# Kernel tuning notes

Measured on AMD Instinct MI355X. Metric: run time of the kernel, lower is better.

Reference implementation:

```python
import jax, jax.numpy as jnp
import numpy as np
from jax import lax

L, H = 16384, 1024
EPS = 1e-5


def _ln(x, w, b):
    m = jnp.mean(x, axis=-1, keepdims=True)
    v = jnp.var(x, axis=-1, keepdims=True)
    return (x - m) * lax.rsqrt(v + EPS) * w + b


def setup_inputs() -> dict:
    key = jax.random.key(0)
    ks = jax.random.split(key, 12)
    s = 0.02
    return {
        "x": jax.random.normal(ks[0], (L, H), dtype=jnp.float32),
        "ln1_w": jnp.ones((H,), jnp.float32),
        "ln1_b": jnp.zeros((H,), jnp.float32),
        "W_in": jax.random.normal(ks[1], (H, H), jnp.float32) * s,
        "b_in": jnp.zeros((H,), jnp.float32),
        "W_gate": jax.random.normal(ks[2], (H, H), jnp.float32) * s,
        "b_gate": jnp.zeros((H,), jnp.float32),
        "W_out": jax.random.normal(ks[3], (H, H), jnp.float32) * s,
        "b_out": jnp.zeros((H,), jnp.float32),
        "state_decay": jnp.zeros((H,), jnp.float32),
        "ln2_w": jnp.ones((H,), jnp.float32),
        "ln2_b": jnp.zeros((H,), jnp.float32),
        "W_ff1": jax.random.normal(ks[4], (H, 2 * H), jnp.float32) * s,
        "b_ff1": jnp.zeros((2 * H,), jnp.float32),
        "W_ff2": jax.random.normal(ks[5], (2 * H, H), jnp.float32) * s,
        "b_ff2": jnp.zeros((H,), jnp.float32),
    }


def reference(x, ln1_w, ln1_b, W_in, b_in, W_gate, b_gate, W_out, b_out,
              state_decay, ln2_w, ln2_b, W_ff1, b_ff1, W_ff2, b_ff2):
    hidden = _ln(x, ln1_w, ln1_b)                       # [L,H]
    u = hidden @ W_in + b_in                            # [L,H]
    gate = jax.nn.sigmoid(hidden @ W_gate + b_gate)     # [L,H]
    decay = jax.nn.sigmoid(state_decay)                 # [H]

    def step(s, u_t):
        s = decay * s + u_t
        return s, s

    z = jnp.zeros((x.shape[1],), x.dtype)
    _, states_f = lax.scan(step, z, u)                  # forward recurrence
    _, states_b = lax.scan(step, z, u, reverse=True)    # backward recurrence
    state_out = 0.5 * (states_f + states_b) * gate

    x = x + state_out @ W_out + b_out
    h = _ln(x, ln2_w, ln2_b)
    x = x + jax.nn.silu(h @ W_ff1 + b_ff1) @ W_ff2 + b_ff2
    return x
```

## Files before the change

kernel.cpp:

```cpp
#include <hip/hip_runtime.h>
#include <hip/hip_bf16.h>
#include <hip/hip_fp16.h>

#define L_SEQ 16384
#define HDIM  1024
#define CH    32
#define NC    (L_SEQ / CH)

typedef _Float16 f16;
typedef _Float16 f16x8 __attribute__((ext_vector_type(8)));
typedef _Float16 f16x4 __attribute__((ext_vector_type(4)));
typedef float    f32x4 __attribute__((ext_vector_type(4)));

#define AS1(p) (const __attribute__((address_space(1))) void*)(p)
#define AS3(p) (__attribute__((address_space(3))) void*)(p)

__global__ __launch_bounds__(256) void wcvt_t(const float* __restrict__ in,
                                              f16* __restrict__ out, int K, int N) {
  __shared__ float tile[32][33];
  int n0 = blockIdx.x * 32, k0 = blockIdx.y * 32;
  int tx = threadIdx.x, ty = threadIdx.y;
#pragma unroll
  for (int i = 0; i < 4; i++) {
    int k = k0 + ty + i * 8;
    tile[ty + i * 8][tx] = in[(size_t)k * N + n0 + tx];
  }
  __syncthreads();
#pragma unroll
  for (int i = 0; i < 4; i++) {
    int n = n0 + ty + i * 8;
    out[(size_t)n * K + k0 + tx] = (f16)tile[tx][ty + i * 8];
  }
}

__global__ __launch_bounds__(256) void ln_k(const float* __restrict__ x,
                                            const float* __restrict__ w,
                                            const float* __restrict__ b,
                                            f16* __restrict__ out,
                                            f16* __restrict__ xcopy) {
  int row = blockIdx.x;
  int t = threadIdx.x;
  const float4* xr = (const float4*)(x + (size_t)row * HDIM);
  float4 v = xr[t];
  float s  = v.x + v.y + v.z + v.w;
  float s2 = v.x * v.x + v.y * v.y + v.z * v.z + v.w * v.w;
#pragma unroll
  for (int off = 32; off > 0; off >>= 1) {
    s  += __shfl_down(s, off);
    s2 += __shfl_down(s2, off);
  }
  __shared__ float red[8];
  int wid = t >> 6, lane = t & 63;
  if (lane == 0) { red[wid] = s; red[4 + wid] = s2; }
  __syncthreads();
  if (t == 0) {
    red[0] = red[0] + red[1] + red[2] + red[3];
    red[4] = red[4] + red[5] + red[6] + red[7];
  }
  __syncthreads();
  float mean = red[0] * (1.0f / HDIM);
  float var  = red[4] * (1.0f / HDIM) - mean * mean;
  float rstd = rsqrtf(var + 1e-5f);
  float4 ww = ((const float4*)w)[t];
  float4 bb = ((const float4*)b)[t];
  f16x4 o;
  o[0] = (f16)((v.x - mean) * rstd * ww.x + bb.x);
  o[1] = (f16)((v.y - mean) * rstd * ww.y + bb.y);
  o[2] = (f16)((v.z - mean) * rstd * ww.z + bb.z);
  o[3] = (f16)((v.w - mean) * rstd * ww.w + bb.w);
  ((f16x4*)(out + (size_t)row * HDIM))[t] = o;
  if (xcopy) {
    f16x4 c;
    c[0] = (f16)v.x; c[1] = (f16)v.y; c[2] = (f16)v.z; c[3] = (f16)v.w;
    ((f16x4*)(xcopy + (size_t)row * HDIM))[t] = c;
  }
}

__global__ __launch_bounds__(128) void ln_k16(const f16* __restrict__ x,
                                              const float* __restrict__ w,
                                              const float* __restrict__ b,
                                              f16* __restrict__ out) {
  int row = blockIdx.x;
  int t = threadIdx.x;
  f16x8 xv = ((const f16x8*)(x + (size_t)row * HDIM))[t];
  float v[8];
  float s = 0.f, s2 = 0.f;
#pragma unroll
  for (int i = 0; i < 8; i++) {
    v[i] = (float)xv[i];
    s += v[i]; s2 += v[i] * v[i];
  }
#pragma unroll
  for (int off = 32; off > 0; off >>= 1) {
    s  += __shfl_down(s, off);
    s2 += __shfl_down(s2, off);
  }
  __shared__ float red[4];
  int wid = t >> 6, lane = t & 63;
  if (lane == 0) { red[wid] = s; red[2 + wid] = s2; }
  __syncthreads();
  float mean = (red[0] + red[1]) * (1.0f / HDIM);
  float var  = (red[2] + red[3]) * (1.0f / HDIM) - mean * mean;
  float rstd = rsqrtf(var + 1e-5f);
  float4 w1 = ((const float4*)w)[2 * t], w2 = ((const float4*)w)[2 * t + 1];
  float4 b1 = ((const float4*)b)[2 * t], b2 = ((const float4*)b)[2 * t + 1];
  float wv[8] = {w1.x, w1.y, w1.z, w1.w, w2.x, w2.y, w2.z, w2.w};
  float bv[8] = {b1.x, b1.y, b1.z, b1.w, b2.x, b2.y, b2.z, b2.w};
  f16x8 o;
#pragma unroll
  for (int i = 0; i < 8; i++) o[i] = (f16)((v[i] - mean) * rstd * wv[i] + bv[i]);
  ((f16x8*)(out + (size_t)row * HDIM))[t] = o;
}

template <int MODE, int RESID, int OUTF16>
__global__ __launch_bounds__(256, 4) void gemm_bt(const f16* __restrict__ A,
                                                  const f16* __restrict__ BT,
                                                  const float* __restrict__ bias,
                                                  const float* __restrict__ bias2,
                                                  const f16* __restrict__ resid,
                                                  void* __restrict__ Cout,
                                                  void* __restrict__ Cout2,
                                                  int M, int N, int K) {
  __shared__ __align__(16) f16 As[2][128 * 32];
  __shared__ __align__(16) f16 Bs[2][128 * 32];
  const int tid  = threadIdx.x;
  const int lane = tid & 63, wid = tid >> 6;
  const int wm = wid >> 1, wn = wid & 1;
  const int quad = lane >> 4, l16 = lane & 15;

  const int nbx = N >> 7, nby = M >> 7;
  const int b = blockIdx.x;
  const int xcd = b & 7;
  const int i = b >> 3;
  const int strips = nby >> 3;
  const int rs = i / nbx, cb = i - rs * nbx;
  const long m0 = (long)(xcd * strips + rs) << 7;
  const long n0 = (long)cb << 7;

  const int srow = wid * 16 + (lane >> 2);
  const int scol = (lane & 3) * 8;
  const f16* gA = A  + (m0 + srow) * K + scol;
  const f16* gB = BT + (n0 + srow) * K + scol;
  const int sdst = wid * 1024;

  f32x4 zero = {0.f, 0.f, 0.f, 0.f};
  f32x4 acc[4][4];
#pragma unroll
  for (int i2 = 0; i2 < 4; i2++)
#pragma unroll
    for (int j = 0; j < 4; j++) acc[i2][j] = zero;

#pragma unroll
  for (int it = 0; it < 2; ++it) {
    __builtin_amdgcn_global_load_lds(AS1(gA + (size_t)(it * 64) * K),
                                     AS3((char*)As[0] + it * 4096 + sdst), 16, 0, 0);
    __builtin_amdgcn_global_load_lds(AS1(gB + (size_t)(it * 64) * K),
                                     AS3((char*)Bs[0] + it * 4096 + sdst), 16, 0, 0);
  }
  __syncthreads();

  const int niter = K >> 5;
  for (int ki = 0; ki < niter; ++ki) {
    const int cur = ki & 1;
    if (ki + 1 < niter) {
      const int nxt = cur ^ 1;
      const int koff = (ki + 1) << 5;
#pragma unroll
      for (int it = 0; it < 2; ++it) {
        __builtin_amdgcn_global_load_lds(AS1(gA + (size_t)(it * 64) * K + koff),
                                         AS3((char*)As[nxt] + it * 4096 + sdst), 16, 0, 0);
        __builtin_amdgcn_global_load_lds(AS1(gB + (size_t)(it * 64) * K + koff),
                                         AS3((char*)Bs[nxt] + it * 4096 + sdst), 16, 0, 0);
      }
    }
    f16x8 af[4], bfr[4];
#pragma unroll
    for (int mi = 0; mi < 4; ++mi)
      af[mi] = *(const f16x8*)(As[cur] + (wm * 64 + mi * 16 + l16) * 32 + quad * 8);
#pragma unroll
    for (int ni = 0; ni < 4; ++ni)
      bfr[ni] = *(const f16x8*)(Bs[cur] + (wn * 64 + ni * 16 + l16) * 32 + quad * 8);
#pragma unroll
    for (int mi = 0; mi < 4; ++mi)
#pragma unroll
      for (int ni = 0; ni < 4; ++ni)
        acc[mi][ni] = __builtin_amdgcn_mfma_f32_16x16x32_f16(af[mi], bfr[ni], acc[mi][ni], 0, 0, 0);
    __syncthreads();
  }

#pragma unroll
  for (int mi = 0; mi < 4; ++mi) {
#pragma unroll
    for (int ni = 0; ni < 4; ++ni) {
      const long col = n0 + wn * 64 + ni * 16 + l16;
      float bc;
      if (MODE == 3) bc = (col < HDIM) ? bias[col] : bias2[col - HDIM];
      else           bc = bias[col];
#pragma unroll
      for (int r = 0; r < 4; ++r) {
        const long row = m0 + wm * 64 + mi * 16 + quad * 4 + r;
        float v = acc[mi][ni][r] + bc;
        if (MODE == 2) v = v / (1.f + __expf(-v));
        if (MODE == 3) {
          if (col < HDIM) {
            ((f16*)Cout)[row * HDIM + col] = (f16)v;
          } else {
            float g = 1.f / (1.f + __expf(-v));
            ((f16*)Cout2)[row * HDIM + (col - HDIM)] = (f16)g;
          }
        } else {
          if (RESID) v += (float)resid[row * N + col];
          if (OUTF16) ((f16*)Cout)[row * N + col] = (f16)v;
          else        ((float*)Cout)[row * N + col] = v;
        }
      }
    }
  }
}

__global__ __launch_bounds__(256) void scan_p1(const f16* __restrict__ u,
                                               const float* __restrict__ sdecay,
                                               float* __restrict__ carry_f,
                                               float* __restrict__ carry_b) {
  int tid = blockIdx.x * 256 + threadIdx.x;
  int h = tid & (HDIM - 1);
  int c = tid >> 10;
  float d = 1.f / (1.f + expf(-sdecay[h]));
  const f16* up = u + (size_t)c * CH * HDIM + h;
  float sf = 0.f, sb = 0.f, p = 1.f;
#pragma unroll
  for (int i = 0; i < CH; i++) {
    float uu = (float)up[i * HDIM];
    sf = d * sf + uu;
    sb += p * uu;
    p *= d;
  }
  carry_f[(size_t)c * HDIM + h] = sf;
  carry_b[(size_t)c * HDIM + h] = sb;
}

__global__ __launch_bounds__(256) void scan_p2(const float* __restrict__ sdecay,
                                               const float* __restrict__ carry_f,
                                               const float* __restrict__ carry_b,
                                               float* __restrict__ cin_f,
                                               float* __restrict__ cin_b) {
  int tid = blockIdx.x * 256 + threadIdx.x;
  int h = tid & (HDIM - 1);
  int dir = tid >> 10;
  float d = 1.f / (1.f + expf(-sdecay[h]));
  float dT = powf(d, (float)CH);
  float S = 0.f;
  if (dir == 0) {
#pragma unroll 4
    for (int c = 0; c < NC; c++) {
      cin_f[(size_t)c * HDIM + h] = S;
      S = dT * S + carry_f[(size_t)c * HDIM + h];
    }
  } else {
#pragma unroll 4
    for (int c = NC - 1; c >= 0; c--) {
      cin_b[(size_t)c * HDIM + h] = S;
      S = dT * S + carry_b[(size_t)c * HDIM + h];
    }
  }
}

__global__ __launch_bounds__(256) void scan_p3(const f16* __restrict__ u,
                                               const f16* __restrict__ gate,
                                               const float* __restrict__ sdecay,
                                               const float* __restrict__ cin_f,
                                               const float* __restrict__ cin_b,
                                               f16* __restrict__ state_out) {
  int tid = blockIdx.x * 256 + threadIdx.x;
  int h = tid & (HDIM - 1);
  int c = tid >> 10;
  float d = 1.f / (1.f + expf(-sdecay[h]));
  const f16* up = u    + (size_t)c * CH * HDIM + h;
  const f16* gp = gate + (size_t)c * CH * HDIM + h;
  f16* op = state_out  + (size_t)c * CH * HDIM + h;
  float ur[CH], sf[CH];
#pragma unroll
  for (int i = 0; i < CH; i++) ur[i] = (float)up[i * HDIM];
  float s = cin_f[(size_t)c * HDIM + h];
#pragma unroll
  for (int i = 0; i < CH; i++) { s = d * s + ur[i]; sf[i] = s; }
  s = cin_b[(size_t)c * HDIM + h];
#pragma unroll
  for (int i = CH - 1; i >= 0; i--) {
    s = d * s + ur[i];
    float g = (float)gp[i * HDIM];
    op[i * HDIM] = (f16)(0.5f * (sf[i] + s) * g);
  }
}

extern "C" void kernel_launch(void* const* d_in, const int* in_sizes, int n_in,
                              void* d_out, int out_size, void* d_ws, size_t ws_size,
                              hipStream_t stream) {
  const float* x      = (const float*)d_in[0];
  const float* ln1_w  = (const float*)d_in[1];
  const float* ln1_b  = (const float*)d_in[2];
  const float* W_in   = (const float*)d_in[3];
  const float* b_in   = (const float*)d_in[4];
  const float* W_gate = (const float*)d_in[5];
  const float* b_gate = (const float*)d_in[6];
  const float* W_out  = (const float*)d_in[7];
  const float* b_out  = (const float*)d_in[8];
  const float* sdecay = (const float*)d_in[9];
  const float* ln2_w  = (const float*)d_in[10];
  const float* ln2_b  = (const float*)d_in[11];
  const float* W_ff1  = (const float*)d_in[12];
  const float* b_ff1  = (const float*)d_in[13];
  const float* W_ff2  = (const float*)d_in[14];
  const float* b_ff2  = (const float*)d_in[15];
  float* out = (float*)d_out;

  char* ws = (char*)d_ws;
  const size_t MB32 = 33554432, MB64 = 67108864;
  f16* hidden = (f16*)(ws);
  f16* xh     = (f16*)(ws + MB32);
  f16* u      = (f16*)(ws + 2 * MB32);
  f16* gate   = (f16*)(ws + 3 * MB32);
  f16* x2h    = (f16*)(ws + 4 * MB32);
  f16* ff     = (f16*)(ws + 5 * MB32);
  char* wbase = ws + 5 * MB32 + MB64;
  f16* wt_ug  = (f16*)(wbase);
  f16* wt_out = (f16*)(wbase + 4194304);
  f16* wt_ff1 = (f16*)(wbase + 4194304 + 2097152);
  f16* wt_ff2 = (f16*)(wbase + 2 * 4194304 + 2097152);
  char* cbase = wbase + 3 * 4194304 + 2097152;
  float* carry_f = (float*)(cbase);
  float* carry_b = (float*)(cbase + 2097152);
  float* cin_f   = (float*)(cbase + 2 * 2097152);
  float* cin_b   = (float*)(cbase + 3 * 2097152);
  f16* state_out = hidden;
  f16* h2        = u;

  dim3 tb(32, 8);
  wcvt_t<<<dim3(32, 32), tb, 0, stream>>>(W_in,   wt_ug,                 1024, 1024);
  wcvt_t<<<dim3(32, 32), tb, 0, stream>>>(W_gate, wt_ug + 1024 * 1024,   1024, 1024);
  wcvt_t<<<dim3(32, 32), tb, 0, stream>>>(W_out,  wt_out,                1024, 1024);
  wcvt_t<<<dim3(64, 32), tb, 0, stream>>>(W_ff1,  wt_ff1,                1024, 2048);
  wcvt_t<<<dim3(32, 64), tb, 0, stream>>>(W_ff2,  wt_ff2,                2048, 1024);

  ln_k<<<L_SEQ, 256, 0, stream>>>(x, ln1_w, ln1_b, hidden, xh);

  gemm_bt<3, 0, 1><<<2048, 256, 0, stream>>>(hidden, wt_ug, b_in, b_gate, nullptr,
                                             u, gate, L_SEQ, 2048, 1024);

  scan_p1<<<2048, 256, 0, stream>>>(u, sdecay, carry_f, carry_b);
  scan_p2<<<8, 256, 0, stream>>>(sdecay, carry_f, carry_b, cin_f, cin_b);
  scan_p3<<<2048, 256, 0, stream>>>(u, gate, sdecay, cin_f, cin_b, state_out);

  gemm_bt<0, 1, 1><<<1024, 256, 0, stream>>>(state_out, wt_out, b_out, nullptr, xh,
                                             x2h, nullptr, L_SEQ, 1024, 1024);

  ln_k16<<<L_SEQ, 128, 0, stream>>>(x2h, ln2_w, ln2_b, h2);

  gemm_bt<2, 0, 1><<<2048, 256, 0, stream>>>(h2, wt_ff1, b_ff1, nullptr, nullptr,
                                             ff, nullptr, L_SEQ, 2048, 1024);

  gemm_bt<0, 1, 0><<<1024, 256, 0, stream>>>(ff, wt_ff2, b_ff2, nullptr, x2h,
                                             out, nullptr, L_SEQ, 1024, 2048);
}
```

Measured before the change: 613.5 us.

## Replace 128x128 GEMM with 256x256 tile, 4-stage LDS ring and swizzle

Replaces the double-buffered 128x128 GEMM with a 512-thread 256x256 tile kernel that keeps a 4-deep LDS ring, prefetching three K-slices ahead with explicit vmcnt waits and barriers. LDS layout is XOR-swizzled to reduce bank conflicts, and MFMA phases are bracketed with setprio/sched_barrier so loads interleave with compute. The aim is higher data reuse per global byte and better latency hiding. The trade-off is fewer blocks (one wave on 256 CUs for N=1024 GEMMs), large LDS footprint limiting occupancy, and more registers for the 8x4 accumulators.

```diff
diff --git a/kernel.cpp b/kernel.cpp
--- a/kernel.cpp
+++ b/kernel.cpp
@@ -112,8 +112,72 @@
   ((f16x8*)(out + (size_t)row * HDIM))[t] = o;
 }
 
+
+template <int VM, bool STAGE>
+__device__ __forceinline__ void tile256(int t, int K,
+                                        const f16* __restrict__ gAs,
+                                        const f16* __restrict__ gBs,
+                                        f16 (*sA)[8192], f16 (*sB)[8192],
+                                        int wid, int wm, int wn, int l16, int quad,
+                                        f32x4 (&acc)[8][4]) {
+  const int cur = t & 3;
+  if constexpr (VM == 8)      asm volatile("s_waitcnt vmcnt(8)" ::: "memory");
+  else if constexpr (VM == 4) asm volatile("s_waitcnt vmcnt(4)" ::: "memory");
+  else                        asm volatile("s_waitcnt vmcnt(0)" ::: "memory");
+  __builtin_amdgcn_s_barrier();
+
+  const f16* Ab = sA[cur];
+  const f16* Bb = sB[cur];
+  f16x8 afr[4], bfr[4];
+#pragma unroll
+  for (int i = 0; i < 4; ++i) {
+    const int ar = wm * 128 + i * 16 + l16;
+    afr[i] = *(const f16x8*)(Ab + ar * 32 + ((quad ^ ((ar >> 1) & 3)) << 3));
+    const int br = wn * 64 + i * 16 + l16;
+    bfr[i] = *(const f16x8*)(Bb + br * 32 + ((quad ^ ((br >> 1) & 3)) << 3));
+  }
+  if constexpr (STAGE) {
+    const int nb = (t + 3) & 3;
+#pragma unroll
+    for (int r = 0; r < 2; ++r)
+      __builtin_amdgcn_global_load_lds(AS1(gAs + (size_t)r * 128 * K + (size_t)(t + 3) * 32),
+                                       AS3((char*)sA[nb] + r * 8192 + wid * 1024), 16, 0, 0);
+  }
+  __builtin_amdgcn_s_barrier();
+  __builtin_amdgcn_sched_barrier(0);
+  __builtin_amdgcn_s_setprio(1);
+#pragma unroll
+  for (int mi = 0; mi < 4; ++mi)
+#pragma unroll
+    for (int ni = 0; ni < 4; ++ni)
+      acc[mi][ni] = __builtin_amdgcn_mfma_f32_16x16x32_f16(afr[mi], bfr[ni], acc[mi][ni], 0, 0, 0);
+  __builtin_amdgcn_s_setprio(0);
+  __builtin_amdgcn_sched_barrier(0);
+  __builtin_amdgcn_s_barrier();
+#pragma unroll
+  for (int i = 0; i < 4; ++i) {
+    const int ar = wm * 128 + (4 + i) * 16 + l16;
+    afr[i] = *(const f16x8*)(Ab + ar * 32 + ((quad ^ ((ar >> 1) & 3)) << 3));
+  }
+  if constexpr (STAGE) {
+    const int nb = (t + 3) & 3;
+#pragma unroll
+    for (int r = 0; r < 2; ++r)
+      __builtin_amdgcn_global_load_lds(AS1(gBs + (size_t)r * 128 * K + (size_t)(t + 3) * 32),
+                                       AS3((char*)sB[nb] + r * 8192 + wid * 1024), 16, 0, 0);
+  }
+  __builtin_amdgcn_sched_barrier(0);
+  __builtin_amdgcn_s_setprio(1);
+#pragma unroll
+  for (int mi = 0; mi < 4; ++mi)
+#pragma unroll
+    for (int ni = 0; ni < 4; ++ni)
+      acc[4 + mi][ni] = __builtin_amdgcn_mfma_f32_16x16x32_f16(afr[mi], bfr[ni], acc[4 + mi][ni], 0, 0, 0);
+  __builtin_amdgcn_s_setprio(0);
+}
+
 template <int MODE, int RESID, int OUTF16>
-__global__ __launch_bounds__(256, 4) void gemm_bt(const f16* __restrict__ A,
+__global__ __launch_bounds__(512, 2) void gemm256(const f16* __restrict__ A,
                                                   const f16* __restrict__ BT,
                                                   const float* __restrict__ bias,
                                                   const float* __restrict__ bias2,
@@ -121,75 +185,56 @@
                                                   void* __restrict__ Cout,
                                                   void* __restrict__ Cout2,
                                                   int M, int N, int K) {
-  __shared__ __align__(16) f16 As[2][128 * 32];
-  __shared__ __align__(16) f16 Bs[2][128 * 32];
+  __shared__ __align__(16) f16 sA[4][8192];
+  __shared__ __align__(16) f16 sB[4][8192];
   const int tid  = threadIdx.x;
   const int lane = tid & 63, wid = tid >> 6;
-  const int wm = wid >> 1, wn = wid & 1;
+  const int wm = wid >> 2, wn = wid & 3;
   const int quad = lane >> 4, l16 = lane & 15;
 
-  const int nbx = N >> 7, nby = M >> 7;
+  const int nbx = N >> 8, nby = M >> 8;
   const int b = blockIdx.x;
   const int xcd = b & 7;
   const int i = b >> 3;
   const int strips = nby >> 3;
   const int rs = i / nbx, cb = i - rs * nbx;
-  const long m0 = (long)(xcd * strips + rs) << 7;
-  const long n0 = (long)cb << 7;
-
-  const int srow = wid * 16 + (lane >> 2);
-  const int scol = (lane & 3) * 8;
-  const f16* gA = A  + (m0 + srow) * K + scol;
-  const f16* gB = BT + (n0 + srow) * K + scol;
-  const int sdst = wid * 1024;
+  const long m0 = (long)(xcd * strips + rs) << 8;
+  const long n0 = (long)cb << 8;
+
+  const int row_s = tid >> 2;
+  const int qa = (tid & 3) ^ ((row_s >> 1) & 3);
+  const f16* gAs = A  + (size_t)(m0 + row_s) * K + qa * 8;
+  const f16* gBs = BT + (size_t)(n0 + row_s) * K + qa * 8;
 
   f32x4 zero = {0.f, 0.f, 0.f, 0.f};
-  f32x4 acc[4][4];
-#pragma unroll
-  for (int i2 = 0; i2 < 4; i2++)
-#pragma unroll
-    for (int j = 0; j < 4; j++) acc[i2][j] = zero;
-
-#pragma unroll
-  for (int it = 0; it < 2; ++it) {
-    __builtin_amdgcn_global_load_lds(AS1(gA + (size_t)(it * 64) * K),
-                                     AS3((char*)As[0] + it * 4096 + sdst), 16, 0, 0);
-    __builtin_amdgcn_global_load_lds(AS1(gB + (size_t)(it * 64) * K),
-                                     AS3((char*)Bs[0] + it * 4096 + sdst), 16, 0, 0);
-  }
-  __syncthreads();
-
-  const int niter = K >> 5;
-  for (int ki = 0; ki < niter; ++ki) {
-    const int cur = ki & 1;
-    if (ki + 1 < niter) {
-      const int nxt = cur ^ 1;
-      const int koff = (ki + 1) << 5;
-#pragma unroll
-      for (int it = 0; it < 2; ++it) {
-        __builtin_amdgcn_global_load_lds(AS1(gA + (size_t)(it * 64) * K + koff),
-                                         AS3((char*)As[nxt] + it * 4096 + sdst), 16, 0, 0);
-        __builtin_amdgcn_global_load_lds(AS1(gB + (size_t)(it * 64) * K + koff),
-                                         AS3((char*)Bs[nxt] + it * 4096 + sdst), 16, 0, 0);
-      }
-    }
-    f16x8 af[4], bfr[4];
-#pragma unroll
-    for (int mi = 0; mi < 4; ++mi)
-      af[mi] = *(const f16x8*)(As[cur] + (wm * 64 + mi * 16 + l16) * 32 + quad * 8);
-#pragma unroll
-    for (int ni = 0; ni < 4; ++ni)
-      bfr[ni] = *(const f16x8*)(Bs[cur] + (wn * 64 + ni * 16 + l16) * 32 + quad * 8);
-#pragma unroll
-    for (int mi = 0; mi < 4; ++mi)
-#pragma unroll
-      for (int ni = 0; ni < 4; ++ni)
-        acc[mi][ni] = __builtin_amdgcn_mfma_f32_16x16x32_f16(af[mi], bfr[ni], acc[mi][ni], 0, 0, 0);
-    __syncthreads();
-  }
-
-#pragma unroll
-  for (int mi = 0; mi < 4; ++mi) {
+  f32x4 acc[8][4];
+#pragma unroll
+  for (int mi = 0; mi < 8; ++mi)
+#pragma unroll
+    for (int ni = 0; ni < 4; ++ni) acc[mi][ni] = zero;
+
+#pragma unroll
+  for (int pt = 0; pt < 3; ++pt) {
+#pragma unroll
+    for (int r = 0; r < 2; ++r)
+      __builtin_amdgcn_global_load_lds(AS1(gAs + (size_t)r * 128 * K + (size_t)pt * 32),
+                                       AS3((char*)sA[pt] + r * 8192 + wid * 1024), 16, 0, 0);
+#pragma unroll
+    for (int r = 0; r < 2; ++r)
+      __builtin_amdgcn_global_load_lds(AS1(gBs + (size_t)r * 128 * K + (size_t)pt * 32),
+                                       AS3((char*)sB[pt] + r * 8192 + wid * 1024), 16, 0, 0);
+  }
+
+  const int nt = K >> 5;
+  int t = 0;
+  for (; t < nt - 3; ++t)
+    tile256<8, true >(t, K, gAs, gBs, sA, sB, wid, wm, wn, l16, quad, acc);
+  tile256<8, false>(t, K, gAs, gBs, sA, sB, wid, wm, wn, l16, quad, acc); ++t;
+  tile256<4, false>(t, K, gAs, gBs, sA, sB, wid, wm, wn, l16, quad, acc); ++t;
+  tile256<0, false>(t, K, gAs, gBs, sA, sB, wid, wm, wn, l16, quad, acc);
+
+#pragma unroll
+  for (int mi = 0; mi < 8; ++mi) {
 #pragma unroll
     for (int ni = 0; ni < 4; ++ni) {
       const long col = n0 + wn * 64 + ni * 16 + l16;
@@ -198,7 +243,7 @@
       else           bc = bias[col];
 #pragma unroll
       for (int r = 0; r < 4; ++r) {
-        const long row = m0 + wm * 64 + mi * 16 + quad * 4 + r;
+        const long row = m0 + wm * 128 + mi * 16 + quad * 4 + r;
         float v = acc[mi][ni][r] + bc;
         if (MODE == 2) v = v / (1.f + __expf(-v));
         if (MODE == 3) {
@@ -344,21 +389,21 @@
 
   ln_k<<<L_SEQ, 256, 0, stream>>>(x, ln1_w, ln1_b, hidden, xh);
 
-  gemm_bt<3, 0, 1><<<2048, 256, 0, stream>>>(hidden, wt_ug, b_in, b_gate, nullptr,
-                                             u, gate, L_SEQ, 2048, 1024);
+  gemm256<3, 0, 1><<<512, 512, 0, stream>>>(hidden, wt_ug, b_in, b_gate, nullptr,
+                                            u, gate, L_SEQ, 2048, 1024);
 
   scan_p1<<<2048, 256, 0, stream>>>(u, sdecay, carry_f, carry_b);
   scan_p2<<<8, 256, 0, stream>>>(sdecay, carry_f, carry_b, cin_f, cin_b);
   scan_p3<<<2048, 256, 0, stream>>>(u, gate, sdecay, cin_f, cin_b, state_out);
 
-  gemm_bt<0, 1, 1><<<1024, 256, 0, stream>>>(state_out, wt_out, b_out, nullptr, xh,
-                                             x2h, nullptr, L_SEQ, 1024, 1024);
+  gemm256<0, 1, 1><<<256, 512, 0, stream>>>(state_out, wt_out, b_out, nullptr, xh,
+                                            x2h, nullptr, L_SEQ, 1024, 1024);
 
   ln_k16<<<L_SEQ, 128, 0, stream>>>(x2h, ln2_w, ln2_b, h2);
 
-  gemm_bt<2, 0, 1><<<2048, 256, 0, stream>>>(h2, wt_ff1, b_ff1, nullptr, nullptr,
-                                             ff, nullptr, L_SEQ, 2048, 1024);
-
-  gemm_bt<0, 1, 0><<<1024, 256, 0, stream>>>(ff, wt_ff2, b_ff2, nullptr, x2h,
-                                             out, nullptr, L_SEQ, 1024, 2048);
-}
+  gemm256<2, 0, 1><<<512, 512, 0, stream>>>(h2, wt_ff1, b_ff1, nullptr, nullptr,
+                                            ff, nullptr, L_SEQ, 2048, 1024);
+
+  gemm256<0, 1, 0><<<256, 512, 0, stream>>>(ff, wt_ff2, b_ff2, nullptr, x2h,
+                                            out, nullptr, L_SEQ, 1024, 2048);
+}
```

Result: slower. 679.0 us (+10.7%).
